# Performance work log

Measured on AMD Instinct MI355X. Metric: run time of the kernel, lower is better.

The kernel has to match this reference:

```python
import jax, jax.numpy as jnp
import numpy as np

N, K = 4096, 256          # rays, samples per ray
V = 100000                # voxel table size
D = 64                    # field MLP hidden dim
SCALER = 7.0              # free-energy scaler from the source


def setup_inputs() -> dict:
    key = jax.random.key(0)
    ks = jax.random.split(key, 12)
    ray_start = jax.random.normal(ks[0], (N, 3), jnp.float32)
    rd = jax.random.normal(ks[1], (N, 3), jnp.float32)
    ray_dir = rd / jnp.linalg.norm(rd, axis=-1, keepdims=True)
    sampled_depth = jnp.sort(
        0.5 + 4.0 * jax.random.uniform(ks[2], (N, K), jnp.float32), axis=-1)
    sampled_dists = 0.02 * jax.random.uniform(ks[3], (N, K), jnp.float32)
    raw = jax.random.randint(ks[4], (N, K), 0, V + V // 4)
    sampled_idx = jnp.where(raw < V, raw, -1).astype(jnp.int64)
    voxel_color = 0.1 * jax.random.normal(ks[5], (V, 3), jnp.float32)
    W1 = jax.random.normal(ks[6], (6, D), jnp.float32) * (1.0 / np.sqrt(6.0))
    b1 = jnp.zeros((D,), jnp.float32)
    w_sigma = jax.random.normal(ks[7], (D, 1), jnp.float32) * (1.0 / np.sqrt(D))
    b_sigma = jnp.zeros((1,), jnp.float32)
    W_tex = jax.random.normal(ks[8], (D, 3), jnp.float32) * (1.0 / np.sqrt(D))
    b_tex = jnp.zeros((3,), jnp.float32)
    return dict(ray_start=ray_start, ray_dir=ray_dir,
                sampled_depth=sampled_depth, sampled_dists=sampled_dists,
                sampled_idx=sampled_idx, voxel_color=voxel_color,
                W1=W1, b1=b1, w_sigma=w_sigma, b_sigma=b_sigma,
                W_tex=W_tex, b_tex=b_tex)


def reference(ray_start, ray_dir, sampled_depth, sampled_dists, sampled_idx,
              voxel_color, W1, b1, w_sigma, b_sigma, W_tex, b_tex):
    mask = sampled_idx != -1                                   # [N,K] sample_mask
    # sampled_xyz = ray(start, dir, depth); sampled_dir broadcast of ray_dir
    xyz = ray_start[:, None, :] + ray_dir[:, None, :] * sampled_depth[..., None]
    dirs = jnp.broadcast_to(ray_dir[:, None, :], xyz.shape)    # [N,K,3]
    feat = jnp.concatenate([xyz, dirs], axis=-1)               # [N,K,6]
    # field_fn: small MLP -> sigma, texture
    h = jax.nn.relu(jnp.einsum('nkf,fd->nkd', feat, W1) + b1)  # [N,K,D]
    sigma = (jnp.einsum('nkd,do->nko', h, w_sigma) + b_sigma)[..., 0]  # [N,K]
    # voxel color embedding lookup (F.embedding); res=True adds it to texture
    idx_safe = jnp.where(mask, sampled_idx, 0)
    vcol = voxel_color[idx_safe]                               # [N,K,3] gather
    texture = jnp.einsum('nkd,dc->nkc', h, W_tex) + b_tex + vcol
    # free energy; masked_scatter == zero-out where mask is False
    free_energy = jnp.where(mask,
                            jax.nn.relu(sigma) * sampled_dists * SCALER, 0.0)
    texture = jnp.where(mask[..., None], texture, 0.0)
    # alpha compositing: a = 1-exp(-fe), b = exp(-cumsum(shifted fe))
    shifted = jnp.concatenate(
        [jnp.zeros((free_energy.shape[0], 1), free_energy.dtype),
         free_energy[:, :-1]], axis=-1)
    a = 1.0 - jnp.exp(-free_energy)
    b = jnp.exp(-jnp.cumsum(shifted, axis=-1))
    probs = a * b                                              # [N,K]
    depths = jnp.sum(sampled_depth * probs, axis=-1)           # [N]
    missed = 1.0 - jnp.sum(probs, axis=-1)                     # [N]
    colors = jnp.sum(texture * probs[..., None], axis=-2)      # [N,3]
    return colors, depths, missed, probs
```

## Files before the change

### kernel.cpp

```cpp
#include <hip/hip_runtime.h>

#define K_SAMP 256
#define D_HID 64
#define SCALER_FE 7.0f

typedef _Float16 half8 __attribute__((ext_vector_type(8)));
typedef float f32x4 __attribute__((ext_vector_type(4)));

__device__ __forceinline__ half8 h8zero() {
    half8 a;
    #pragma unroll
    for (int j = 0; j < 8; ++j) a[j] = (_Float16)0.f;
    return a;
}

__global__ __launch_bounds__(256, 4)
void volrend_kernel(const float* __restrict__ ray_start,
                    const float* __restrict__ ray_dir,
                    const float* __restrict__ depth,
                    const float* __restrict__ dists,
                    const int*   __restrict__ vidx,
                    const float* __restrict__ vcol_tab,
                    const float* __restrict__ W1,
                    const float* __restrict__ b1,
                    const float* __restrict__ w_sigma,
                    const float* __restrict__ b_sigma,
                    const float* __restrict__ W_tex,
                    const float* __restrict__ b_tex,
                    float* __restrict__ out_colors,
                    float* __restrict__ out_depths,
                    float* __restrict__ out_missed,
                    float* __restrict__ out_probs) {
    __shared__ float lds[4][K_SAMP][4];

    const int lane = threadIdx.x & 63;
    const int wv   = threadIdx.x >> 6;
    const int ray  = __builtin_amdgcn_readfirstlane(blockIdx.x * 4 + wv);
    const int m    = lane & 15;
    const int g    = lane >> 4;

    const float rs0 = ray_start[ray * 3 + 0];
    const float rs1 = ray_start[ray * 3 + 1];
    const float rs2 = ray_start[ray * 3 + 2];
    const float rd0 = ray_dir[ray * 3 + 0];
    const float rd1 = ray_dir[ray * 3 + 1];
    const float rd2 = ray_dir[ray * 3 + 2];
    const float bs  = b_sigma[0];
    const float bt0 = b_tex[0], bt1 = b_tex[1], bt2 = b_tex[2];

    half8 a1[4];
    #pragma unroll
    for (int tt = 0; tt < 4; ++tt) {
        const int dim = 8 * (m >> 2) + (m & 3) + 4 * (tt & 1) + 32 * (tt >> 1);
        half8 a = h8zero();
        if (g == 0) {
            #pragma unroll
            for (int j = 0; j < 6; ++j) a[j] = (_Float16)W1[j * D_HID + dim];
            a[6] = (_Float16)b1[dim];
        }
        a1[tt] = a;
    }

    half8 a2a = h8zero(), a2b = h8zero();
    if (m < 4) {
        const int c = (m >= 1) ? (m - 1) : 0;
        #pragma unroll
        for (int j = 0; j < 8; ++j) {
            const int d = 8 * g + j;
            const float va = (m == 0) ? w_sigma[d]      : W_tex[d * 3 + c];
            const float vb = (m == 0) ? w_sigma[d + 32] : W_tex[(d + 32) * 3 + c];
            a2a[j] = (_Float16)va;
            a2b[j] = (_Float16)vb;
        }
    }

    const size_t rayBase = (size_t)ray * K_SAMP;
    const float4 dep = ((const float4*)(depth + rayBase))[lane];
    const float4 dst = ((const float4*)(dists + rayBase))[lane];
    const int4   vi  = ((const int4*)(vidx  + rayBase))[lane];
    const float depa[4] = {dep.x, dep.y, dep.z, dep.w};
    const float dsta[4] = {dst.x, dst.y, dst.z, dst.w};
    const int   via[4]  = {vi.x, vi.y, vi.z, vi.w};
    float vc[4][3];
    bool  msk[4];
    #pragma unroll
    for (int s = 0; s < 4; ++s) {
        msk[s] = (via[s] != -1);
        const int b = (msk[s] ? via[s] : 0) * 3;
        vc[s][0] = vcol_tab[b + 0];
        vc[s][1] = vcol_tab[b + 1];
        vc[s][2] = vcol_tab[b + 2];
    }

    f32x4 oinit = {0.f, 0.f, 0.f, 0.f};
    if (g == 0) { oinit[0] = bs; oinit[1] = bt0; oinit[2] = bt1; oinit[3] = bt2; }
    const f32x4 zero4 = {0.f, 0.f, 0.f, 0.f};

    #pragma unroll 2
    for (int t = 0; t < 16; ++t) {
        const float dpt = depth[rayBase + 16 * t + m];
        const float fx = fmaf(rd0, dpt, rs0);
        const float fy = fmaf(rd1, dpt, rs1);
        const float fz = fmaf(rd2, dpt, rs2);
        half8 b1f = h8zero();
        if (g == 0) {
            b1f[0] = (_Float16)fx;  b1f[1] = (_Float16)fy;  b1f[2] = (_Float16)fz;
            b1f[3] = (_Float16)rd0; b1f[4] = (_Float16)rd1; b1f[5] = (_Float16)rd2;
            b1f[6] = (_Float16)1.0f;
        }
        f32x4 h0 = __builtin_amdgcn_mfma_f32_16x16x32_f16(a1[0], b1f, zero4, 0, 0, 0);
        f32x4 h1 = __builtin_amdgcn_mfma_f32_16x16x32_f16(a1[1], b1f, zero4, 0, 0, 0);
        f32x4 h2 = __builtin_amdgcn_mfma_f32_16x16x32_f16(a1[2], b1f, zero4, 0, 0, 0);
        f32x4 h3 = __builtin_amdgcn_mfma_f32_16x16x32_f16(a1[3], b1f, zero4, 0, 0, 0);

        half8 b2a, b2b;
        #pragma unroll
        for (int r = 0; r < 4; ++r) {
            b2a[r]     = (_Float16)fmaxf(h0[r], 0.f);
            b2a[r + 4] = (_Float16)fmaxf(h1[r], 0.f);
            b2b[r]     = (_Float16)fmaxf(h2[r], 0.f);
            b2b[r + 4] = (_Float16)fmaxf(h3[r], 0.f);
        }
        f32x4 o = oinit;
        o = __builtin_amdgcn_mfma_f32_16x16x32_f16(a2a, b2a, o, 0, 0, 0);
        o = __builtin_amdgcn_mfma_f32_16x16x32_f16(a2b, b2b, o, 0, 0, 0);

        if (g == 0) {
            *(float4*)&lds[wv][16 * t + m][0] = make_float4(o[0], o[1], o[2], o[3]);
        }
    }
    __syncthreads();

    float sg[4], tA[4], tB[4], tC[4];
    #pragma unroll
    for (int c = 0; c < 4; ++c) {
        const float4 r = *(const float4*)&lds[wv][4 * lane + c][0];
        sg[c] = r.x; tA[c] = r.y; tB[c] = r.z; tC[c] = r.w;
    }

    float fe[4];
    #pragma unroll
    for (int s = 0; s < 4; ++s) {
        if (msk[s]) {
            fe[s] = fmaxf(sg[s], 0.0f) * dsta[s] * SCALER_FE;
            tA[s] += vc[s][0];
            tB[s] += vc[s][1];
            tC[s] += vc[s][2];
        } else {
            fe[s] = 0.0f;
            tA[s] = 0.0f; tB[s] = 0.0f; tC[s] = 0.0f;
        }
    }

    const float T = fe[0] + fe[1] + fe[2] + fe[3];
    float x = T;
    #pragma unroll
    for (int off = 1; off < 64; off <<= 1) {
        float v = __shfl_up(x, off, 64);
        if (lane >= off) x += v;
    }
    float e0 = x - T;
    float e1 = e0 + fe[0];
    float e2 = e1 + fe[1];
    float e3 = e2 + fe[2];

    const float p0 = (1.0f - __expf(-fe[0])) * __expf(-e0);
    const float p1 = (1.0f - __expf(-fe[1])) * __expf(-e1);
    const float p2 = (1.0f - __expf(-fe[2])) * __expf(-e2);
    const float p3 = (1.0f - __expf(-fe[3])) * __expf(-e3);

    float sp = p0 + p1 + p2 + p3;
    float sd = depa[0] * p0 + depa[1] * p1 + depa[2] * p2 + depa[3] * p3;
    float c0 = tA[0] * p0 + tA[1] * p1 + tA[2] * p2 + tA[3] * p3;
    float c1 = tB[0] * p0 + tB[1] * p1 + tB[2] * p2 + tB[3] * p3;
    float c2 = tC[0] * p0 + tC[1] * p1 + tC[2] * p2 + tC[3] * p3;
    #pragma unroll
    for (int off = 32; off > 0; off >>= 1) {
        sp += __shfl_down(sp, off, 64);
        sd += __shfl_down(sd, off, 64);
        c0 += __shfl_down(c0, off, 64);
        c1 += __shfl_down(c1, off, 64);
        c2 += __shfl_down(c2, off, 64);
    }
    if (lane == 0) {
        out_colors[ray * 3 + 0] = c0;
        out_colors[ray * 3 + 1] = c1;
        out_colors[ray * 3 + 2] = c2;
        out_depths[ray] = sd;
        out_missed[ray] = 1.0f - sp;
    }
    ((float4*)(out_probs + rayBase))[lane] = make_float4(p0, p1, p2, p3);
}

extern "C" void kernel_launch(void* const* d_in, const int* in_sizes, int n_in,
                              void* d_out, int out_size, void* d_ws, size_t ws_size,
                              hipStream_t stream) {
    const float* ray_start  = (const float*)d_in[0];
    const float* ray_dir    = (const float*)d_in[1];
    const float* depth      = (const float*)d_in[2];
    const float* dists      = (const float*)d_in[3];
    const int*   vidx       = (const int*)d_in[4];
    const float* vcol       = (const float*)d_in[5];
    const float* W1         = (const float*)d_in[6];
    const float* b1         = (const float*)d_in[7];
    const float* w_sigma    = (const float*)d_in[8];
    const float* b_sigma    = (const float*)d_in[9];
    const float* W_tex      = (const float*)d_in[10];
    const float* b_tex      = (const float*)d_in[11];

    const int N = in_sizes[0] / 3;
    float* out        = (float*)d_out;
    float* out_colors = out;
    float* out_depths = out + (size_t)N * 3;
    float* out_missed = out + (size_t)N * 3 + N;
    float* out_probs  = out + (size_t)N * 3 + 2 * (size_t)N;

    volrend_kernel<<<N / 4, 256, 0, stream>>>(
        ray_start, ray_dir, depth, dists, vidx, vcol,
        W1, b1, w_sigma, b_sigma, W_tex, b_tex,
        out_colors, out_depths, out_missed, out_probs);
}
```

Baseline: 21.92 us.

## Split each ray across two waves with cross-wave scan carry and reduction

Each ray is now handled by two wavefronts, each taking 128 samples, so the grid doubles to N/2 blocks of 256 threads. This roughly halves the serial MFMA loop per wave and raises occupancy through a higher launch-bounds minimum-blocks hint. The per-sample loads and the voxel-colour gather now happen after the MLP loop. Cross-wave transmittance is carried through a shared prefix total, and the final sums are combined in shared memory. The cost is two block-wide barriers plus duplicated weight-fragment setup per wave.

```diff
diff --git a/kernel.cpp b/kernel.cpp
--- a/kernel.cpp
+++ b/kernel.cpp
@@ -14,7 +14,7 @@
     return a;
 }
 
-__global__ __launch_bounds__(256, 4)
+__global__ __launch_bounds__(256, 8)
 void volrend_kernel(const float* __restrict__ ray_start,
                     const float* __restrict__ ray_dir,
                     const float* __restrict__ depth,
@@ -31,11 +31,15 @@
                     float* __restrict__ out_depths,
                     float* __restrict__ out_missed,
                     float* __restrict__ out_probs) {
-    __shared__ float lds[4][K_SAMP][4];
+    __shared__ float sOut[2][K_SAMP][4];
+    __shared__ float sHtot[2];
+    __shared__ float sRed[2][2][5];
 
     const int lane = threadIdx.x & 63;
     const int wv   = threadIdx.x >> 6;
-    const int ray  = __builtin_amdgcn_readfirstlane(blockIdx.x * 4 + wv);
+    const int r    = wv >> 1;
+    const int half = __builtin_amdgcn_readfirstlane(wv & 1);
+    const int ray  = __builtin_amdgcn_readfirstlane(blockIdx.x * 2 + r);
     const int m    = lane & 15;
     const int g    = lane >> 4;
 
@@ -74,31 +78,16 @@
         }
     }
 
-    const size_t rayBase = (size_t)ray * K_SAMP;
-    const float4 dep = ((const float4*)(depth + rayBase))[lane];
-    const float4 dst = ((const float4*)(dists + rayBase))[lane];
-    const int4   vi  = ((const int4*)(vidx  + rayBase))[lane];
-    const float depa[4] = {dep.x, dep.y, dep.z, dep.w};
-    const float dsta[4] = {dst.x, dst.y, dst.z, dst.w};
-    const int   via[4]  = {vi.x, vi.y, vi.z, vi.w};
-    float vc[4][3];
-    bool  msk[4];
-    #pragma unroll
-    for (int s = 0; s < 4; ++s) {
-        msk[s] = (via[s] != -1);
-        const int b = (msk[s] ? via[s] : 0) * 3;
-        vc[s][0] = vcol_tab[b + 0];
-        vc[s][1] = vcol_tab[b + 1];
-        vc[s][2] = vcol_tab[b + 2];
-    }
-
     f32x4 oinit = {0.f, 0.f, 0.f, 0.f};
     if (g == 0) { oinit[0] = bs; oinit[1] = bt0; oinit[2] = bt1; oinit[3] = bt2; }
     const f32x4 zero4 = {0.f, 0.f, 0.f, 0.f};
 
+    const size_t rayBase  = (size_t)ray * K_SAMP;
+    const size_t halfBase = rayBase + half * 128;
+
     #pragma unroll 2
-    for (int t = 0; t < 16; ++t) {
-        const float dpt = depth[rayBase + 16 * t + m];
+    for (int t = 0; t < 8; ++t) {
+        const float dpt = depth[halfBase + 16 * t + m];
         const float fx = fmaf(rd0, dpt, rs0);
         const float fy = fmaf(rd1, dpt, rs1);
         const float fz = fmaf(rd2, dpt, rs2);
@@ -115,65 +104,70 @@
 
         half8 b2a, b2b;
         #pragma unroll
-        for (int r = 0; r < 4; ++r) {
-            b2a[r]     = (_Float16)fmaxf(h0[r], 0.f);
-            b2a[r + 4] = (_Float16)fmaxf(h1[r], 0.f);
-            b2b[r]     = (_Float16)fmaxf(h2[r], 0.f);
-            b2b[r + 4] = (_Float16)fmaxf(h3[r], 0.f);
+        for (int rr = 0; rr < 4; ++rr) {
+            b2a[rr]     = (_Float16)fmaxf(h0[rr], 0.f);
+            b2a[rr + 4] = (_Float16)fmaxf(h1[rr], 0.f);
+            b2b[rr]     = (_Float16)fmaxf(h2[rr], 0.f);
+            b2b[rr + 4] = (_Float16)fmaxf(h3[rr], 0.f);
         }
         f32x4 o = oinit;
         o = __builtin_amdgcn_mfma_f32_16x16x32_f16(a2a, b2a, o, 0, 0, 0);
         o = __builtin_amdgcn_mfma_f32_16x16x32_f16(a2b, b2b, o, 0, 0, 0);
 
         if (g == 0) {
-            *(float4*)&lds[wv][16 * t + m][0] = make_float4(o[0], o[1], o[2], o[3]);
-        }
-    }
-    __syncthreads();
-
-    float sg[4], tA[4], tB[4], tC[4];
-    #pragma unroll
-    for (int c = 0; c < 4; ++c) {
-        const float4 r = *(const float4*)&lds[wv][4 * lane + c][0];
-        sg[c] = r.x; tA[c] = r.y; tB[c] = r.z; tC[c] = r.w;
-    }
-
-    float fe[4];
-    #pragma unroll
-    for (int s = 0; s < 4; ++s) {
-        if (msk[s]) {
-            fe[s] = fmaxf(sg[s], 0.0f) * dsta[s] * SCALER_FE;
-            tA[s] += vc[s][0];
-            tB[s] += vc[s][1];
-            tC[s] += vc[s][2];
-        } else {
-            fe[s] = 0.0f;
-            tA[s] = 0.0f; tB[s] = 0.0f; tC[s] = 0.0f;
-        }
-    }
-
-    const float T = fe[0] + fe[1] + fe[2] + fe[3];
+            *(float4*)&sOut[r][half * 128 + 16 * t + m][0] =
+                make_float4(o[0], o[1], o[2], o[3]);
+        }
+    }
+
+    const float2 dep = ((const float2*)(depth + halfBase))[lane];
+    const float2 dst = ((const float2*)(dists + halfBase))[lane];
+    const int2   vi  = ((const int2*)(vidx  + halfBase))[lane];
+    const bool msk0 = (vi.x != -1);
+    const bool msk1 = (vi.y != -1);
+    const int  vb0  = (msk0 ? vi.x : 0) * 3;
+    const int  vb1  = (msk1 ? vi.y : 0) * 3;
+    const float vcx0 = vcol_tab[vb0 + 0], vcy0 = vcol_tab[vb0 + 1], vcz0 = vcol_tab[vb0 + 2];
+    const float vcx1 = vcol_tab[vb1 + 0], vcy1 = vcol_tab[vb1 + 1], vcz1 = vcol_tab[vb1 + 2];
+
+    const int sIdx = half * 128 + 2 * lane;
+    const float4 r0 = *(const float4*)&sOut[r][sIdx][0];
+    const float4 r1 = *(const float4*)&sOut[r][sIdx + 1][0];
+
+    float fe0 = 0.f, fe1 = 0.f;
+    float tA0 = 0.f, tB0 = 0.f, tC0 = 0.f;
+    float tA1 = 0.f, tB1 = 0.f, tC1 = 0.f;
+    if (msk0) {
+        fe0 = fmaxf(r0.x, 0.f) * dst.x * SCALER_FE;
+        tA0 = r0.y + vcx0; tB0 = r0.z + vcy0; tC0 = r0.w + vcz0;
+    }
+    if (msk1) {
+        fe1 = fmaxf(r1.x, 0.f) * dst.y * SCALER_FE;
+        tA1 = r1.y + vcx1; tB1 = r1.z + vcy1; tC1 = r1.w + vcz1;
+    }
+
+    const float T = fe0 + fe1;
     float x = T;
     #pragma unroll
     for (int off = 1; off < 64; off <<= 1) {
         float v = __shfl_up(x, off, 64);
         if (lane >= off) x += v;
     }
-    float e0 = x - T;
-    float e1 = e0 + fe[0];
-    float e2 = e1 + fe[1];
-    float e3 = e2 + fe[2];
-
-    const float p0 = (1.0f - __expf(-fe[0])) * __expf(-e0);
-    const float p1 = (1.0f - __expf(-fe[1])) * __expf(-e1);
-    const float p2 = (1.0f - __expf(-fe[2])) * __expf(-e2);
-    const float p3 = (1.0f - __expf(-fe[3])) * __expf(-e3);
-
-    float sp = p0 + p1 + p2 + p3;
-    float sd = depa[0] * p0 + depa[1] * p1 + depa[2] * p2 + depa[3] * p3;
-    float c0 = tA[0] * p0 + tA[1] * p1 + tA[2] * p2 + tA[3] * p3;
-    float c1 = tB[0] * p0 + tB[1] * p1 + tB[2] * p2 + tB[3] * p3;
-    float c2 = tC[0] * p0 + tC[1] * p1 + tC[2] * p2 + tC[3] * p3;
+    if (half == 0 && lane == 63) sHtot[r] = x;
+    __syncthreads();
+
+    const float base = half ? sHtot[r] : 0.0f;
+    const float e0 = base + x - T;
+    const float e1 = e0 + fe0;
+
+    const float p0 = (1.0f - __expf(-fe0)) * __expf(-e0);
+    const float p1 = (1.0f - __expf(-fe1)) * __expf(-e1);
+
+    float sp = p0 + p1;
+    float sd = dep.x * p0 + dep.y * p1;
+    float c0 = tA0 * p0 + tA1 * p1;
+    float c1 = tB0 * p0 + tB1 * p1;
+    float c2 = tC0 * p0 + tC1 * p1;
     #pragma unroll
     for (int off = 32; off > 0; off >>= 1) {
         sp += __shfl_down(sp, off, 64);
@@ -183,13 +177,28 @@
         c2 += __shfl_down(c2, off, 64);
     }
     if (lane == 0) {
-        out_colors[ray * 3 + 0] = c0;
-        out_colors[ray * 3 + 1] = c1;
-        out_colors[ray * 3 + 2] = c2;
-        out_depths[ray] = sd;
-        out_missed[ray] = 1.0f - sp;
-    }
-    ((float4*)(out_probs + rayBase))[lane] = make_float4(p0, p1, p2, p3);
+        sRed[r][half][0] = sp;
+        sRed[r][half][1] = sd;
+        sRed[r][half][2] = c0;
+        sRed[r][half][3] = c1;
+        sRed[r][half][4] = c2;
+    }
+
+    ((float2*)(out_probs + halfBase))[lane] = make_float2(p0, p1);
+
+    __syncthreads();
+    if (half == 0 && lane == 0) {
+        const float tp  = sRed[r][0][0] + sRed[r][1][0];
+        const float td  = sRed[r][0][1] + sRed[r][1][1];
+        const float tc0 = sRed[r][0][2] + sRed[r][1][2];
+        const float tc1 = sRed[r][0][3] + sRed[r][1][3];
+        const float tc2 = sRed[r][0][4] + sRed[r][1][4];
+        out_colors[ray * 3 + 0] = tc0;
+        out_colors[ray * 3 + 1] = tc1;
+        out_colors[ray * 3 + 2] = tc2;
+        out_depths[ray] = td;
+        out_missed[ray] = 1.0f - tp;
+    }
 }
 
 extern "C" void kernel_launch(void* const* d_in, const int* in_sizes, int n_in,
@@ -215,7 +224,7 @@
     float* out_missed = out + (size_t)N * 3 + N;
     float* out_probs  = out + (size_t)N * 3 + 2 * (size_t)N;
 
-    volrend_kernel<<<N / 4, 256, 0, stream>>>(
+    volrend_kernel<<<N / 2, 256, 0, stream>>>(
         ray_start, ray_dir, depth, dists, vidx, vcol,
         W1, b1, w_sigma, b_sigma, W_tex, b_tex,
         out_colors, out_depths, out_missed, out_probs);
```

Measured after the change: 21.09 us. 3.8% less time.

## Assign one ray per block, split samples across waves with cross-wave scan

Applied to the files above, without the earlier changes.

Each ray now gets a 256-thread block, and each wave handles 64 of its samples, where before each wave processed a whole ray. That gives 4x more blocks and a quarter of the serial MLP loop per wave. The prefix sum and the final reductions now cross waves through LDS and extra barriers. Weight fragments are built once per block by one wave and shared through LDS. The fp16 packing uses cvt_pkrtz instead of per-element conversions, and the launch-bounds occupancy target is raised. The risks are the added syncthreads, redundant per-wave ray loads, and a change of rounding mode to round-toward-zero.

```diff
diff --git a/kernel.cpp b/kernel.cpp
--- a/kernel.cpp
+++ b/kernel.cpp
@@ -4,8 +4,12 @@
 #define D_HID 64
 #define SCALER_FE 7.0f
 
-typedef _Float16 half8 __attribute__((ext_vector_type(8)));
-typedef float f32x4 __attribute__((ext_vector_type(4)));
+typedef _Float16 half8  __attribute__((ext_vector_type(8)));
+typedef __fp16   fp16x2 __attribute__((ext_vector_type(2)));
+typedef float    f32x4  __attribute__((ext_vector_type(4)));
+
+union H8U4 { half8 h; uint4 u; };
+union H8P  { fp16x2 h2[4]; half8 h8; };
 
 __device__ __forceinline__ half8 h8zero() {
     half8 a;
@@ -14,7 +18,7 @@
     return a;
 }
 
-__global__ __launch_bounds__(256, 4)
+__global__ __launch_bounds__(256, 6)
 void volrend_kernel(const float* __restrict__ ray_start,
                     const float* __restrict__ ray_dir,
                     const float* __restrict__ depth,
@@ -31,13 +35,44 @@
                     float* __restrict__ out_depths,
                     float* __restrict__ out_missed,
                     float* __restrict__ out_probs) {
-    __shared__ float lds[4][K_SAMP][4];
-
-    const int lane = threadIdx.x & 63;
-    const int wv   = threadIdx.x >> 6;
-    const int ray  = __builtin_amdgcn_readfirstlane(blockIdx.x * 4 + wv);
+    __shared__ uint4 sFrag[6 * 64];
+    __shared__ float sOut[K_SAMP][4];
+    __shared__ float sTot[4];
+    __shared__ float sRed[4][5];
+
+    const int tid  = threadIdx.x;
+    const int lane = tid & 63;
+    const int wv   = tid >> 6;
+    const int ray  = blockIdx.x;
     const int m    = lane & 15;
     const int g    = lane >> 4;
+
+    if (tid < 64) {
+        #pragma unroll
+        for (int tt = 0; tt < 4; ++tt) {
+            const int dim = 8 * (m >> 2) + (m & 3) + 4 * (tt & 1) + 32 * (tt >> 1);
+            half8 a = h8zero();
+            if (g == 0) {
+                #pragma unroll
+                for (int j = 0; j < 6; ++j) a[j] = (_Float16)W1[j * D_HID + dim];
+                a[6] = (_Float16)b1[dim];
+            }
+            H8U4 c; c.h = a;
+            sFrag[tt * 64 + lane] = c.u;
+        }
+        half8 a2a = h8zero(), a2b = h8zero();
+        if (m < 4) {
+            const int c = (m >= 1) ? (m - 1) : 0;
+            #pragma unroll
+            for (int j = 0; j < 8; ++j) {
+                const int d = 8 * g + j;
+                a2a[j] = (_Float16)((m == 0) ? w_sigma[d]      : W_tex[d * 3 + c]);
+                a2b[j] = (_Float16)((m == 0) ? w_sigma[d + 32] : W_tex[(d + 32) * 3 + c]);
+            }
+        }
+        H8U4 ca; ca.h = a2a; sFrag[4 * 64 + lane] = ca.u;
+        H8U4 cb; cb.h = a2b; sFrag[5 * 64 + lane] = cb.u;
+    }
 
     const float rs0 = ray_start[ray * 3 + 0];
     const float rs1 = ray_start[ray * 3 + 1];
@@ -48,132 +83,98 @@
     const float bs  = b_sigma[0];
     const float bt0 = b_tex[0], bt1 = b_tex[1], bt2 = b_tex[2];
 
+    __syncthreads();
+
     half8 a1[4];
     #pragma unroll
-    for (int tt = 0; tt < 4; ++tt) {
-        const int dim = 8 * (m >> 2) + (m & 3) + 4 * (tt & 1) + 32 * (tt >> 1);
-        half8 a = h8zero();
-        if (g == 0) {
-            #pragma unroll
-            for (int j = 0; j < 6; ++j) a[j] = (_Float16)W1[j * D_HID + dim];
-            a[6] = (_Float16)b1[dim];
-        }
-        a1[tt] = a;
-    }
-
-    half8 a2a = h8zero(), a2b = h8zero();
-    if (m < 4) {
-        const int c = (m >= 1) ? (m - 1) : 0;
-        #pragma unroll
-        for (int j = 0; j < 8; ++j) {
-            const int d = 8 * g + j;
-            const float va = (m == 0) ? w_sigma[d]      : W_tex[d * 3 + c];
-            const float vb = (m == 0) ? w_sigma[d + 32] : W_tex[(d + 32) * 3 + c];
-            a2a[j] = (_Float16)va;
-            a2b[j] = (_Float16)vb;
-        }
-    }
-
-    const size_t rayBase = (size_t)ray * K_SAMP;
-    const float4 dep = ((const float4*)(depth + rayBase))[lane];
-    const float4 dst = ((const float4*)(dists + rayBase))[lane];
-    const int4   vi  = ((const int4*)(vidx  + rayBase))[lane];
-    const float depa[4] = {dep.x, dep.y, dep.z, dep.w};
-    const float dsta[4] = {dst.x, dst.y, dst.z, dst.w};
-    const int   via[4]  = {vi.x, vi.y, vi.z, vi.w};
-    float vc[4][3];
-    bool  msk[4];
-    #pragma unroll
-    for (int s = 0; s < 4; ++s) {
-        msk[s] = (via[s] != -1);
-        const int b = (msk[s] ? via[s] : 0) * 3;
-        vc[s][0] = vcol_tab[b + 0];
-        vc[s][1] = vcol_tab[b + 1];
-        vc[s][2] = vcol_tab[b + 2];
-    }
+    for (int tt = 0; tt < 4; ++tt) { H8U4 c; c.u = sFrag[tt * 64 + lane]; a1[tt] = c.h; }
+    H8U4 ca; ca.u = sFrag[4 * 64 + lane]; const half8 a2a = ca.h;
+    H8U4 cb; cb.u = sFrag[5 * 64 + lane]; const half8 a2b = cb.h;
 
     f32x4 oinit = {0.f, 0.f, 0.f, 0.f};
     if (g == 0) { oinit[0] = bs; oinit[1] = bt0; oinit[2] = bt1; oinit[3] = bt2; }
     const f32x4 zero4 = {0.f, 0.f, 0.f, 0.f};
 
-    #pragma unroll 2
-    for (int t = 0; t < 16; ++t) {
-        const float dpt = depth[rayBase + 16 * t + m];
+    const fp16x2 hc12 = __builtin_amdgcn_cvt_pkrtz(rd1, rd2);
+    const fp16x2 hc3  = __builtin_amdgcn_cvt_pkrtz(1.0f, 0.0f);
+
+    const size_t rayBase = (size_t)ray * K_SAMP;
+    const int    qBase   = wv * 64;
+
+    #pragma unroll
+    for (int t = 0; t < 4; ++t) {
+        const float dpt = depth[rayBase + qBase + 16 * t + m];
         const float fx = fmaf(rd0, dpt, rs0);
         const float fy = fmaf(rd1, dpt, rs1);
         const float fz = fmaf(rd2, dpt, rs2);
-        half8 b1f = h8zero();
+        H8P bb;
+        bb.h2[0] = __builtin_amdgcn_cvt_pkrtz(fx, fy);
+        bb.h2[1] = __builtin_amdgcn_cvt_pkrtz(fz, rd0);
+        bb.h2[2] = hc12;
+        bb.h2[3] = hc3;
+        const f32x4 h0 = __builtin_amdgcn_mfma_f32_16x16x32_f16(a1[0], bb.h8, zero4, 0, 0, 0);
+        const f32x4 h1 = __builtin_amdgcn_mfma_f32_16x16x32_f16(a1[1], bb.h8, zero4, 0, 0, 0);
+        const f32x4 h2 = __builtin_amdgcn_mfma_f32_16x16x32_f16(a1[2], bb.h8, zero4, 0, 0, 0);
+        const f32x4 h3 = __builtin_amdgcn_mfma_f32_16x16x32_f16(a1[3], bb.h8, zero4, 0, 0, 0);
+
+        H8P p2a, p2b;
+        p2a.h2[0] = __builtin_amdgcn_cvt_pkrtz(fmaxf(h0[0], 0.f), fmaxf(h0[1], 0.f));
+        p2a.h2[1] = __builtin_amdgcn_cvt_pkrtz(fmaxf(h0[2], 0.f), fmaxf(h0[3], 0.f));
+        p2a.h2[2] = __builtin_amdgcn_cvt_pkrtz(fmaxf(h1[0], 0.f), fmaxf(h1[1], 0.f));
+        p2a.h2[3] = __builtin_amdgcn_cvt_pkrtz(fmaxf(h1[2], 0.f), fmaxf(h1[3], 0.f));
+        p2b.h2[0] = __builtin_amdgcn_cvt_pkrtz(fmaxf(h2[0], 0.f), fmaxf(h2[1], 0.f));
+        p2b.h2[1] = __builtin_amdgcn_cvt_pkrtz(fmaxf(h2[2], 0.f), fmaxf(h2[3], 0.f));
+        p2b.h2[2] = __builtin_amdgcn_cvt_pkrtz(fmaxf(h3[0], 0.f), fmaxf(h3[1], 0.f));
+        p2b.h2[3] = __builtin_amdgcn_cvt_pkrtz(fmaxf(h3[2], 0.f), fmaxf(h3[3], 0.f));
+
+        f32x4 o = oinit;
+        o = __builtin_amdgcn_mfma_f32_16x16x32_f16(a2a, p2a.h8, o, 0, 0, 0);
+        o = __builtin_amdgcn_mfma_f32_16x16x32_f16(a2b, p2b.h8, o, 0, 0, 0);
+
         if (g == 0) {
-            b1f[0] = (_Float16)fx;  b1f[1] = (_Float16)fy;  b1f[2] = (_Float16)fz;
-            b1f[3] = (_Float16)rd0; b1f[4] = (_Float16)rd1; b1f[5] = (_Float16)rd2;
-            b1f[6] = (_Float16)1.0f;
+            *(float4*)&sOut[qBase + 16 * t + m][0] = make_float4(o[0], o[1], o[2], o[3]);
         }
-        f32x4 h0 = __builtin_amdgcn_mfma_f32_16x16x32_f16(a1[0], b1f, zero4, 0, 0, 0);
-        f32x4 h1 = __builtin_amdgcn_mfma_f32_16x16x32_f16(a1[1], b1f, zero4, 0, 0, 0);
-        f32x4 h2 = __builtin_amdgcn_mfma_f32_16x16x32_f16(a1[2], b1f, zero4, 0, 0, 0);
-        f32x4 h3 = __builtin_amdgcn_mfma_f32_16x16x32_f16(a1[3], b1f, zero4, 0, 0, 0);
-
-        half8 b2a, b2b;
-        #pragma unroll
-        for (int r = 0; r < 4; ++r) {
-            b2a[r]     = (_Float16)fmaxf(h0[r], 0.f);
-            b2a[r + 4] = (_Float16)fmaxf(h1[r], 0.f);
-            b2b[r]     = (_Float16)fmaxf(h2[r], 0.f);
-            b2b[r + 4] = (_Float16)fmaxf(h3[r], 0.f);
-        }
-        f32x4 o = oinit;
-        o = __builtin_amdgcn_mfma_f32_16x16x32_f16(a2a, b2a, o, 0, 0, 0);
-        o = __builtin_amdgcn_mfma_f32_16x16x32_f16(a2b, b2b, o, 0, 0, 0);
-
-        if (g == 0) {
-            *(float4*)&lds[wv][16 * t + m][0] = make_float4(o[0], o[1], o[2], o[3]);
-        }
-    }
-    __syncthreads();
-
-    float sg[4], tA[4], tB[4], tC[4];
-    #pragma unroll
-    for (int c = 0; c < 4; ++c) {
-        const float4 r = *(const float4*)&lds[wv][4 * lane + c][0];
-        sg[c] = r.x; tA[c] = r.y; tB[c] = r.z; tC[c] = r.w;
-    }
-
-    float fe[4];
-    #pragma unroll
-    for (int s = 0; s < 4; ++s) {
-        if (msk[s]) {
-            fe[s] = fmaxf(sg[s], 0.0f) * dsta[s] * SCALER_FE;
-            tA[s] += vc[s][0];
-            tB[s] += vc[s][1];
-            tC[s] += vc[s][2];
-        } else {
-            fe[s] = 0.0f;
-            tA[s] = 0.0f; tB[s] = 0.0f; tC[s] = 0.0f;
-        }
-    }
-
-    const float T = fe[0] + fe[1] + fe[2] + fe[3];
-    float x = T;
+    }
+    __syncthreads();
+
+    const float dep = depth[rayBase + tid];
+    const float dst = dists[rayBase + tid];
+    const int   vi  = vidx[rayBase + tid];
+    const bool  msk = (vi != -1);
+    const int   vb  = (msk ? vi : 0) * 3;
+    const float vc0 = vcol_tab[vb + 0];
+    const float vc1 = vcol_tab[vb + 1];
+    const float vc2 = vcol_tab[vb + 2];
+
+    const float4 r4 = *(const float4*)&sOut[tid][0];
+    float fe = 0.f, tA = 0.f, tB = 0.f, tC = 0.f;
+    if (msk) {
+        fe = fmaxf(r4.x, 0.f) * dst * SCALER_FE;
+        tA = r4.y + vc0; tB = r4.z + vc1; tC = r4.w + vc2;
+    }
+
+    float x = fe;
     #pragma unroll
     for (int off = 1; off < 64; off <<= 1) {
         float v = __shfl_up(x, off, 64);
         if (lane >= off) x += v;
     }
-    float e0 = x - T;
-    float e1 = e0 + fe[0];
-    float e2 = e1 + fe[1];
-    float e3 = e2 + fe[2];
-
-    const float p0 = (1.0f - __expf(-fe[0])) * __expf(-e0);
-    const float p1 = (1.0f - __expf(-fe[1])) * __expf(-e1);
-    const float p2 = (1.0f - __expf(-fe[2])) * __expf(-e2);
-    const float p3 = (1.0f - __expf(-fe[3])) * __expf(-e3);
-
-    float sp = p0 + p1 + p2 + p3;
-    float sd = depa[0] * p0 + depa[1] * p1 + depa[2] * p2 + depa[3] * p3;
-    float c0 = tA[0] * p0 + tA[1] * p1 + tA[2] * p2 + tA[3] * p3;
-    float c1 = tB[0] * p0 + tB[1] * p1 + tB[2] * p2 + tB[3] * p3;
-    float c2 = tC[0] * p0 + tC[1] * p1 + tC[2] * p2 + tC[3] * p3;
+    if (lane == 63) sTot[wv] = x;
+    __syncthreads();
+    float base = 0.f;
+    #pragma unroll
+    for (int w = 0; w < 3; ++w) {
+        if (w < wv) base += sTot[w];
+    }
+    const float e0 = base + x - fe;
+    const float p  = (1.0f - __expf(-fe)) * __expf(-e0);
+    out_probs[rayBase + tid] = p;
+
+    float sp = p;
+    float sd = dep * p;
+    float c0 = tA * p;
+    float c1 = tB * p;
+    float c2 = tC * p;
     #pragma unroll
     for (int off = 32; off > 0; off >>= 1) {
         sp += __shfl_down(sp, off, 64);
@@ -183,13 +184,19 @@
         c2 += __shfl_down(c2, off, 64);
     }
     if (lane == 0) {
-        out_colors[ray * 3 + 0] = c0;
-        out_colors[ray * 3 + 1] = c1;
-        out_colors[ray * 3 + 2] = c2;
-        out_depths[ray] = sd;
-        out_missed[ray] = 1.0f - sp;
-    }
-    ((float4*)(out_probs + rayBase))[lane] = make_float4(p0, p1, p2, p3);
+        sRed[wv][0] = sp;
+        sRed[wv][1] = sd;
+        sRed[wv][2] = c0;
+        sRed[wv][3] = c1;
+        sRed[wv][4] = c2;
+    }
+    __syncthreads();
+    if (tid < 5) {
+        const float v = sRed[0][tid] + sRed[1][tid] + sRed[2][tid] + sRed[3][tid];
+        if (tid == 0)      out_missed[ray] = 1.0f - v;
+        else if (tid == 1) out_depths[ray] = v;
+        else               out_colors[ray * 3 + (tid - 2)] = v;
+    }
 }
 
 extern "C" void kernel_launch(void* const* d_in, const int* in_sizes, int n_in,
@@ -215,7 +222,7 @@
     float* out_missed = out + (size_t)N * 3 + N;
     float* out_probs  = out + (size_t)N * 3 + 2 * (size_t)N;
 
-    volrend_kernel<<<N / 4, 256, 0, stream>>>(
+    volrend_kernel<<<N, 256, 0, stream>>>(
         ray_start, ray_dir, depth, dists, vidx, vcol,
         W1, b1, w_sigma, b_sigma, W_tex, b_tex,
         out_colors, out_depths, out_missed, out_probs);
```

Result: faster. 21.05 us (-4.0%).
